# Kernel tuning notes

Measured on AMD Instinct MI355X. Metric: run time of the kernel, lower is better.

## Reference

```python
import jax, jax.numpy as jnp
import numpy as np

N = 50000
HID = 128
NH = 4
E_RES, E_SEQ, E_KNN = 100000, 100000, 200000
BN_EPS = 1e-5
NEG_SLOPE = 0.2


def _gat(h, src, dst, W, al, ar, resW, b):
    """DGL-style GATConv (eval mode: feat_drop off, residual=True, bias).
    h: (N, in), W/resW: (in, H*out), al/ar: (H, out), b: (H*out,)"""
    Hh, out = al.shape
    feat = (h @ W).reshape(N, Hh, out)                 # (N, H, out)
    el = jnp.sum(feat * al, axis=-1)                   # (N, H)
    er = jnp.sum(feat * ar, axis=-1)                   # (N, H)
    e = jax.nn.leaky_relu(el[src] + er[dst], NEG_SLOPE)  # (E, H)
    # edge softmax over incoming edges of each dst node (numerically stable)
    m = jax.ops.segment_max(e, dst, num_segments=N)    # (N, H)
    ex = jnp.exp(e - m[dst])
    s = jax.ops.segment_sum(ex, dst, num_segments=N)
    a = ex / s[dst]                                    # (E, H)
    msg = a[:, :, None] * feat[src]                    # (E, H, out)
    rst = jax.ops.segment_sum(msg, dst, num_segments=N)  # (N, H, out)
    return rst + (h @ resW).reshape(N, Hh, out) + b.reshape(1, Hh, out)


def _hetero(h, src_res, dst_res, src_seq, dst_seq, src_knn, dst_knn, W, al, ar, resW, b):
    # HeteroGraphConv with aggregate='sum' over relations, then mean over heads
    r = _gat(h, src_res, dst_res, W[0], al[0], ar[0], resW[0], b[0])
    r = r + _gat(h, src_seq, dst_seq, W[1], al[1], ar[1], resW[1], b[1])
    r = r + _gat(h, src_knn, dst_knn, W[2], al[2], ar[2], resW[2], b[2])
    return jnp.mean(r, axis=1)                         # (N, out)


def setup_inputs() -> dict:
    key = jax.random.key(0)
    ks = iter(jax.random.split(key, 32))
    inp = {}
    inp["x"] = jax.random.normal(next(ks), (N, HID), jnp.float32)
    inp["src_res"] = jax.random.randint(next(ks), (E_RES,), 0, N, jnp.int32)
    inp["dst_res"] = jax.random.randint(next(ks), (E_RES,), 0, N, jnp.int32)
    inp["src_seq"] = jax.random.randint(next(ks), (E_SEQ,), 0, N, jnp.int32)
    inp["dst_seq"] = jax.random.randint(next(ks), (E_SEQ,), 0, N, jnp.int32)
    inp["src_knn"] = jax.random.randint(next(ks), (E_KNN,), 0, N, jnp.int32)
    inp["dst_knn"] = jax.random.randint(next(ks), (E_KNN,), 0, N, jnp.int32)
    sc = 0.05
    for l in (0, 1):
        inp[f"W{l}"] = jax.random.normal(next(ks), (3, HID, NH * HID), jnp.float32) * sc
        inp[f"al{l}"] = jax.random.normal(next(ks), (3, NH, HID), jnp.float32) * sc
        inp[f"ar{l}"] = jax.random.normal(next(ks), (3, NH, HID), jnp.float32) * sc
        inp[f"resW{l}"] = jax.random.normal(next(ks), (3, HID, NH * HID), jnp.float32) * sc
        inp[f"b{l}"] = jax.random.normal(next(ks), (3, NH * HID), jnp.float32) * sc
    inp["fc_W"] = jax.random.normal(next(ks), (HID, HID), jnp.float32) * sc
    inp["fc_b"] = jax.random.normal(next(ks), (HID,), jnp.float32) * sc
    inp["bn_gamma"] = jnp.ones((HID,), jnp.float32)
    inp["bn_beta"] = jnp.zeros((HID,), jnp.float32)
    inp["bn_mean"] = jax.random.normal(next(ks), (HID,), jnp.float32) * sc
    inp["bn_var"] = jax.random.uniform(next(ks), (HID,), jnp.float32)
    return inp


def reference(x, src_res, dst_res, src_seq, dst_seq, src_knn, dst_knn,
              W0, al0, ar0, resW0, b0, W1, al1, ar1, resW1, b1,
              fc_W, fc_b, bn_gamma, bn_beta, bn_mean, bn_var):
    # layer 0: hetero GAT, head-mean, fc + ReLU + BatchNorm (eval), dropout=identity
    h = _hetero(x, src_res, dst_res, src_seq, dst_seq, src_knn, dst_knn,
                W0, al0, ar0, resW0, b0)
    h = jax.nn.relu(h @ fc_W + fc_b)
    h = (h - bn_mean) / jnp.sqrt(bn_var + BN_EPS) * bn_gamma + bn_beta
    # layer 1 (final): hetero GAT, head-mean
    out = _hetero(h, src_res, dst_res, src_seq, dst_seq, src_knn, dst_knn,
                  W1, al1, ar1, resW1, b1)
    return out
```

## Files before the change

kernel.cpp:

```cpp
#include <hip/hip_runtime.h>
#include <hip/hip_bf16.h>
#include <math.h>
#include <stdint.h>

#define NNODES 50000
#define SCHUNK 4096
#define AW 1664
#define XOFF 1536

typedef __bf16 bf16x8 __attribute__((ext_vector_type(8)));
typedef float f32x4 __attribute__((ext_vector_type(4)));
typedef unsigned short u16;
typedef unsigned int u32;

__device__ __forceinline__ float lrelu(float x){ return x >= 0.f ? x : 0.2f*x; }
__device__ __forceinline__ float lo2f(u32 v){ union{ u32 i; float f; } c; c.i = v<<16; return c.f; }
__device__ __forceinline__ float hi2f(u32 v){ union{ u32 i; float f; } c; c.i = v & 0xffff0000u; return c.f; }
__device__ __forceinline__ u16 f2b(float f){ __hip_bfloat16 h = __float2bfloat16(f); return *(u16*)&h; }
__device__ __forceinline__ u32 packbf(float a, float b){ return (u32)f2b(a) | ((u32)f2b(b) << 16); }

#define GLDS16(g, l) __builtin_amdgcn_global_load_lds( \
    (const __attribute__((address_space(1))) void*)(g), \
    (__attribute__((address_space(3))) void*)(l), 16, 0, 0)

__global__ void prep_all(const float* __restrict__ W0, const float* __restrict__ W1,
                         const float* __restrict__ resW0, const float* __restrict__ resW1,
                         const float* __restrict__ b0, const float* __restrict__ b1,
                         const float* __restrict__ al0, const float* __restrict__ ar0,
                         const float* __restrict__ al1, const float* __restrict__ ar1,
                         const float* __restrict__ fcW,
                         u16* __restrict__ Btb, float* __restrict__ biasf,
                         u16* __restrict__ wlb, u16* __restrict__ fcWtb)
{
    int gid = blockIdx.x*blockDim.x + threadIdx.x;
    if (gid < 2*128*AW){
        int l = gid / (128*AW);
        int rem = gid - l*(128*AW);
        int c = rem / AW;
        int j = rem - c*AW;
        const float* W  = l ? W1 : W0;
        const float* rw = l ? resW1 : resW0;
        float v;
        if (j < XOFF){
            int r = j >> 9, h = (j >> 7) & 3, k = j & 127;
            v = 0.25f * W[(size_t)r*65536 + (size_t)k*512 + h*128 + c];
        } else {
            int k = j - XOFF;
            float s = 0.f;
            for (int r = 0; r < 3; ++r)
                for (int h = 0; h < 4; ++h)
                    s += rw[(size_t)r*65536 + (size_t)k*512 + h*128 + c];
            v = 0.25f * s;
        }
        Btb[gid] = f2b(v);
    }
    if (gid < 256){
        int l = gid >> 7, c = gid & 127;
        const float* bb = l ? b1 : b0;
        float s = 0.f;
        for (int r = 0; r < 3; ++r)
            for (int h = 0; h < 4; ++h)
                s += bb[r*512 + h*128 + c];
        biasf[gid] = 0.25f*s;
    }
    if (gid < 2*128*128){
        int l = gid >> 14;
        int col = (gid >> 7) & 127;
        int k = gid & 127;
        float v = 0.f;
        if (col < 24){
            int r = col >> 3, lr = (col >> 2) & 1, h = col & 3;
            const float* W = l ? W1 : W0;
            const float* av = l ? (lr ? ar1 : al1) : (lr ? ar0 : al0);
            const float* wrow = W + (size_t)r*65536 + (size_t)k*512 + h*128;
            const float* arow = av + r*512 + h*128;
            for (int cc = 0; cc < 128; ++cc) v += wrow[cc]*arow[cc];
        }
        wlb[gid] = f2b(v);
    }
    if (gid < 128*128){
        int k = gid & 127, n = gid >> 7;
        fcWtb[gid] = f2b(fcW[k*128 + n]);
    }
}

__global__ __launch_bounds__(256) void xprep_kernel(const float* __restrict__ x,
    u16* __restrict__ Ax, const u16* __restrict__ wl, float* __restrict__ el, int M)
{
    __shared__ u16 Xs[64*136];
    __shared__ u16 Ws[32*136];
    const int tid = threadIdx.x;
    const int row0 = blockIdx.x*64;
    #pragma unroll
    for (int p = 0; p < 2; ++p){
        int idx = tid + p*256;
        int c = idx >> 4, kc = (idx & 15)*8;
        float4 v = make_float4(0.f,0.f,0.f,0.f);
        if (c < 24) v = *(const float4*)(wl + c*128 + kc);
        *(float4*)&Ws[c*136 + kc] = v;
    }
    int r = tid >> 2, cq = (tid & 3)*32;
    int grow = row0 + r;
    if (grow < M){
        #pragma unroll
        for (int i = 0; i < 8; ++i){
            float4 v = *(const float4*)(x + (size_t)grow*128 + cq + i*4);
            ushort4 o;
            o.x = f2b(v.x); o.y = f2b(v.y); o.z = f2b(v.z); o.w = f2b(v.w);
            *(ushort4*)(Ax + (size_t)grow*AW + cq + i*4) = o;
            *(ushort4*)&Xs[r*136 + cq + i*4] = o;
        }
    } else {
        ushort4 z; z.x=0; z.y=0; z.z=0; z.w=0;
        #pragma unroll
        for (int i = 0; i < 8; ++i) *(ushort4*)&Xs[r*136 + cq + i*4] = z;
    }
    __syncthreads();
    const int lane = tid & 63, wave = tid >> 6;
    const int r16 = lane & 15, quad = lane >> 4;
    f32x4 acc0 = {}, acc1 = {};
    #pragma unroll
    for (int ks = 0; ks < 4; ++ks){
        int ko = ks*32 + quad*8;
        bf16x8 a  = *(const bf16x8*)&Xs[(wave*16 + r16)*136 + ko];
        bf16x8 b0 = *(const bf16x8*)&Ws[r16*136 + ko];
        bf16x8 b1 = *(const bf16x8*)&Ws[(16 + r16)*136 + ko];
        acc0 = __builtin_amdgcn_mfma_f32_16x16x32_bf16(a, b0, acc0, 0,0,0);
        acc1 = __builtin_amdgcn_mfma_f32_16x16x32_bf16(a, b1, acc1, 0,0,0);
    }
    #pragma unroll
    for (int p = 0; p < 4; ++p){
        int row = row0 + wave*16 + quad*4 + p;
        if (row < M){
            el[(size_t)row*32 + r16] = acc0[p];
            if (r16 < 8) el[(size_t)row*32 + 16 + r16] = acc1[p];
        }
    }
}

__global__ void hist_all(const int* __restrict__ d0, const int* __restrict__ d1,
                         const int* __restrict__ d2, int e0, int e1, int e2,
                         int* __restrict__ cnt)
{
    int g = blockIdx.x*blockDim.x + threadIdx.x;
    if (g >= e0 + e1 + e2) return;
    int rel, idx;
    if (g < e0){ rel = 0; idx = g; }
    else if (g < e0 + e1){ rel = 1; idx = g - e0; }
    else { rel = 2; idx = g - e0 - e1; }
    const int* d = rel == 0 ? d0 : (rel == 1 ? d1 : d2);
    atomicAdd(cnt + (size_t)rel*NNODES + d[idx], 1);
}

__global__ __launch_bounds__(256) void scan_part(const int* __restrict__ cnt_all,
                                                 int* __restrict__ partials, int Nn, int nblk)
{
    int rel = blockIdx.y, blk = blockIdx.x;
    const int* cnt = cnt_all + (size_t)rel*Nn;
    int tid = threadIdx.x;
    int i0 = blk*SCHUNK + tid*16;
    int s = 0;
    #pragma unroll
    for (int k = 0; k < 4; ++k){
        int idx = i0 + k*4;
        if (idx + 3 < Nn){ int4 v = *(const int4*)(cnt + idx); s += v.x+v.y+v.z+v.w; }
        else { for (int j = 0; j < 4; ++j) if (idx+j < Nn) s += cnt[idx+j]; }
    }
    #pragma unroll
    for (int off = 1; off < 64; off <<= 1) s += __shfl_xor(s, off);
    __shared__ int ws[4];
    if ((tid & 63) == 0) ws[tid>>6] = s;
    __syncthreads();
    if (tid == 0) partials[rel*nblk + blk] = ws[0]+ws[1]+ws[2]+ws[3];
}

__global__ __launch_bounds__(256) void scan_write(const int* __restrict__ cnt_all,
                                                  const int* __restrict__ partials,
                                                  int* __restrict__ rp_all, int* __restrict__ cur_all,
                                                  int Nn, int nblk)
{
    int rel = blockIdx.y, blk = blockIdx.x;
    const int* cnt = cnt_all + (size_t)rel*Nn;
    int* rp  = rp_all  + (size_t)rel*(Nn+1);
    int* cur = cur_all + (size_t)rel*Nn;
    int tid = threadIdx.x;
    __shared__ int sOff;
    __shared__ int wsum[4];
    if (tid == 0){
        int o = 0;
        for (int b = 0; b < blk; ++b) o += partials[rel*nblk + b];
        sOff = o;
        if (blk == 0){
            int t = 0;
            for (int b = 0; b < nblk; ++b) t += partials[rel*nblk + b];
            rp[Nn] = t;
        }
    }
    int i0 = blk*SCHUNK + tid*16;
    int v[16];
    int s = 0;
    #pragma unroll
    for (int k = 0; k < 16; ++k){
        int idx = i0 + k;
        v[k] = (idx < Nn) ? cnt[idx] : 0;
        s += v[k];
    }
    int lane = tid & 63;
    int incl = s;
    #pragma unroll
    for (int off = 1; off < 64; off <<= 1){
        int t = __shfl_up(incl, off);
        if (lane >= off) incl += t;
    }
    if (lane == 63) wsum[tid>>6] = incl;
    __syncthreads();
    int woff = 0;
    for (int w = 0; w < (tid>>6); ++w) woff += wsum[w];
    int ex = sOff + woff + incl - s;
    #pragma unroll
    for (int k = 0; k < 16; ++k){
        int idx = i0 + k;
        if (idx < Nn){ rp[idx] = ex; cur[idx] = ex; }
        ex += v[k];
    }
}

__global__ void scatter_all(const int* __restrict__ s0, const int* __restrict__ s1,
                            const int* __restrict__ s2,
                            const int* __restrict__ d0, const int* __restrict__ d1,
                            const int* __restrict__ d2, int e0, int e1, int e2,
                            int* __restrict__ cur, int* __restrict__ colb,
                            int* __restrict__ dste)
{
    int g = blockIdx.x*blockDim.x + threadIdx.x;
    if (g >= e0 + e1 + e2) return;
    int rel, idx, coff;
    if (g < e0){ rel = 0; idx = g; coff = 0; }
    else if (g < e0 + e1){ rel = 1; idx = g - e0; coff = e0; }
    else { rel = 2; idx = g - e0 - e1; coff = e0 + e1; }
    const int* sp = rel == 0 ? s0 : (rel == 1 ? s1 : s2);
    const int* dp = rel == 0 ? d0 : (rel == 1 ? d1 : d2);
    int d = dp[idx];
    int pos = atomicAdd(cur + (size_t)rel*NNODES + d, 1);
    colb[coff + pos] = sp[idx];
    dste[coff + pos] = d;
}

__global__ void wprep(const int* __restrict__ colb, const int* __restrict__ dste,
                      int e0, int e01, int etot,
                      const float* __restrict__ el_all, uint4* __restrict__ rec)
{
    int j = blockIdx.x*blockDim.x + threadIdx.x;
    if (j >= etot) return;
    int rel = (j < e0) ? 0 : ((j < e01) ? 1 : 2);
    int src = colb[j], dst = dste[j];
    float4 es = *(const float4*)(el_all + (size_t)src*32 + rel*8);
    float4 ed = *(const float4*)(el_all + (size_t)dst*32 + rel*8 + 4);
    uint4 o;
    o.x = (u32)src;
    o.y = packbf(__expf(lrelu(es.x + ed.x)), __expf(lrelu(es.y + ed.y)));
    o.z = packbf(__expf(lrelu(es.z + ed.z)), __expf(lrelu(es.w + ed.w)));
    o.w = 0;
    rec[j] = o;
}

__global__ __launch_bounds__(256) void agg3(const int* __restrict__ rowp_all,
    const uint4* __restrict__ rec_all, int e0, int e01,
    const u16* __restrict__ Ax, u16* __restrict__ Abuf, int Nn)
{
    const int rel = blockIdx.y;
    const int tid = threadIdx.x;
    const int o = tid & 15;
    const int n = (blockIdx.x*256 + tid) >> 4;
    if (n >= Nn) return;
    const int* rowp = rowp_all + (size_t)rel*(Nn+1);
    const int coff = (rel == 0) ? 0 : ((rel == 1) ? e0 : e01);
    const uint4* rec = rec_all + coff;
    u16* op = Abuf + (size_t)n*AW + rel*512 + o*8;

    int beg = rowp[n], end = rowp[n+1];
    if (beg >= end){
        uint4 z; z.x = 0; z.y = 0; z.z = 0; z.w = 0;
        #pragma unroll
        for (int h = 0; h < 4; ++h) *(uint4*)(op + h*128) = z;
        return;
    }
    float acc[4][8] = {};
    float us0 = 0.f, us1 = 0.f, us2 = 0.f, us3 = 0.f;

    uint4 ra = rec[beg];
    uint4 xa = *(const uint4*)(Ax + (size_t)ra.x*AW + o*8);
    uint4 rb = ra, xb = xa;
    if (beg + 1 < end){
        rb = rec[beg+1];
        xb = *(const uint4*)(Ax + (size_t)rb.x*AW + o*8);
    }
    for (int j = beg; j < end; ++j){
        uint4 rc = rb, xc = xb;
        if (j + 2 < end){
            rc = rec[j+2];
            xc = *(const uint4*)(Ax + (size_t)rc.x*AW + o*8);
        }
        float w0 = lo2f(ra.y), w1 = hi2f(ra.y), w2 = lo2f(ra.z), w3 = hi2f(ra.z);
        us0 += w0; us1 += w1; us2 += w2; us3 += w3;
        float xv[8];
        xv[0] = lo2f(xa.x); xv[1] = hi2f(xa.x);
        xv[2] = lo2f(xa.y); xv[3] = hi2f(xa.y);
        xv[4] = lo2f(xa.z); xv[5] = hi2f(xa.z);
        xv[6] = lo2f(xa.w); xv[7] = hi2f(xa.w);
        #pragma unroll
        for (int c = 0; c < 8; ++c){
            acc[0][c] = fmaf(w0, xv[c], acc[0][c]);
            acc[1][c] = fmaf(w1, xv[c], acc[1][c]);
            acc[2][c] = fmaf(w2, xv[c], acc[2][c]);
            acc[3][c] = fmaf(w3, xv[c], acc[3][c]);
        }
        ra = rb; xa = xb; rb = rc; xb = xc;
    }
    float inv[4] = {1.f/us0, 1.f/us1, 1.f/us2, 1.f/us3};
    #pragma unroll
    for (int h = 0; h < 4; ++h){
        uint4 ov;
        ov.x = packbf(acc[h][0]*inv[h], acc[h][1]*inv[h]);
        ov.y = packbf(acc[h][2]*inv[h], acc[h][3]*inv[h]);
        ov.z = packbf(acc[h][4]*inv[h], acc[h][5]*inv[h]);
        ov.w = packbf(acc[h][6]*inv[h], acc[h][7]*inv[h]);
        *(uint4*)(op + h*128) = ov;
    }
}

template<int EPI, int FCF>
__global__ __launch_bounds__(256) void gemm_f(
    const u16* __restrict__ A, int Astride, int K,
    const u16* __restrict__ Bt,
    float* __restrict__ Cf, u16* __restrict__ Cb, int Cstride, int M,
    const float* __restrict__ bias, const float* __restrict__ gamma,
    const float* __restrict__ beta, const float* __restrict__ mean,
    const float* __restrict__ var,
    const u16* __restrict__ wl, float* __restrict__ el,
    const u16* __restrict__ fcw, const float* __restrict__ fcb2)
{
    __shared__ u16 smem[26112];
    const int tid = threadIdx.x;
    const int row0 = blockIdx.x*64;
    const int lane = tid & 63, wave = tid >> 6;
    const int wm = (wave >> 1)*32, wn = (wave & 1)*64;
    const int r16 = lane & 15, quad = lane >> 4;
    f32x4 acc[2][4] = {};

    const int r8 = lane >> 3, jc = lane & 7;
    const int soff = ((jc ^ r8) << 3);
    int gA0 = row0 + wave*16 + r8;      if (gA0 >= M) gA0 = M - 1;
    int gA1 = row0 + wave*16 + 8 + r8;  if (gA1 >= M) gA1 = M - 1;
    const u16* srcA0 = A + (size_t)gA0*Astride + soff;
    const u16* srcA1 = A + (size_t)gA1*Astride + soff;
    const u16* srcB0 = Bt + (size_t)(wave*32      + r8)*K + soff;
    const u16* srcB1 = Bt + (size_t)(wave*32 + 8  + r8)*K + soff;
    const u16* srcB2 = Bt + (size_t)(wave*32 + 16 + r8)*K + soff;
    const u16* srcB3 = Bt + (size_t)(wave*32 + 24 + r8)*K + soff;
    const int nk = K >> 6;
    const int swzbase = r16 & 7;

    #define STAGE(buf, k0) do { \
        u16* As_ = smem + (buf)*12288; \
        u16* Bs_ = As_ + 4096; \
        GLDS16(srcA0 + (k0), As_ + wave*1024); \
        GLDS16(srcA1 + (k0), As_ + wave*1024 + 512); \
        GLDS16(srcB0 + (k0), Bs_ + wave*2048); \
        GLDS16(srcB1 + (k0), Bs_ + wave*2048 + 512); \
        GLDS16(srcB2 + (k0), Bs_ + wave*2048 + 1024); \
        GLDS16(srcB3 + (k0), Bs_ + wave*2048 + 1536); \
    } while (0)

    STAGE(0, 0);
    __syncthreads();
    for (int t = 0; t < nk; ++t){
        int cur = t & 1;
        if (t + 1 < nk) STAGE(cur ^ 1, (t + 1) << 6);
        const u16* As = smem + cur*12288;
        const u16* Bs = As + 4096;
        #pragma unroll
        for (int ks = 0; ks < 2; ++ks){
            int swz = ((ks*4 + quad) ^ swzbase) << 3;
            bf16x8 a0 = *(const bf16x8*)&As[(wm + r16)*64 + swz];
            bf16x8 a1 = *(const bf16x8*)&As[(wm + 16 + r16)*64 + swz];
            #pragma unroll
            for (int j = 0; j < 4; ++j){
                bf16x8 b = *(const bf16x8*)&Bs[(wn + j*16 + r16)*64 + swz];
                acc[0][j] = __builtin_amdgcn_mfma_f32_16x16x32_bf16(a0, b, acc[0][j], 0,0,0);
                acc[1][j] = __builtin_amdgcn_mfma_f32_16x16x32_bf16(a1, b, acc[1][j], 0,0,0);
            }
        }
        __syncthreads();
    }
    #undef STAGE

    u16* Cs = smem;
    u16* Ws = smem + 64*136;

    if (!FCF){
        #pragma unroll
        for (int i = 0; i < 2; ++i){
            #pragma unroll
            for (int p = 0; p < 4; ++p){
                int row = row0 + wm + i*16 + quad*4 + p;
                #pragma unroll
                for (int j = 0; j < 4; ++j){
                    int col = wn + j*16 + r16;
                    float v = acc[i][j][p] + bias[col];
                    if (row < M){
                        if (EPI == 1) Cf[(size_t)row*Cstride + col] = v;
                        else          Cb[(size_t)row*Cstride + col] = f2b(v);
                    }
                }
            }
        }
    } else {
        #pragma unroll
        for (int i = 0; i < 2; ++i){
            #pragma unroll
            for (int p = 0; p < 4; ++p){
                int rl = wm + i*16 + quad*4 + p;
                #pragma unroll
                for (int j = 0; j < 4; ++j){
                    int col = wn + j*16 + r16;
                    Cs[rl*136 + col] = f2b(acc[i][j][p] + bias[col]);
                }
            }
        }
        #pragma unroll
        for (int p = 0; p < 8; ++p){
            int idx = tid + p*256;
            int n = idx >> 4, kc = (idx & 15)*8;
            *(float4*)&Ws[n*136 + kc] = *(const float4*)(fcw + n*128 + kc);
        }
        __syncthreads();
        f32x4 fa[8] = {};
        #pragma unroll
        for (int ks = 0; ks < 4; ++ks){
            int ko = ks*32 + quad*8;
            bf16x8 a = *(const bf16x8*)&Cs[(wave*16 + r16)*136 + ko];
            #pragma unroll
            for (int j = 0; j < 8; ++j){
                bf16x8 b = *(const bf16x8*)&Ws[(j*16 + r16)*136 + ko];
                fa[j] = __builtin_amdgcn_mfma_f32_16x16x32_bf16(a, b, fa[j], 0,0,0);
            }
        }
        __syncthreads();
        #pragma unroll
        for (int j = 0; j < 8; ++j){
            int col = j*16 + r16;
            float fb = fcb2[col];
            float mn = mean[col];
            float sc = gamma[col]*rsqrtf(var[col] + 1e-5f);
            float bt = beta[col];
            #pragma unroll
            for (int p = 0; p < 4; ++p){
                int rl = wave*16 + quad*4 + p;
                int row = row0 + rl;
                float v = fa[j][p] + fb;
                v = fmaxf(v, 0.f);
                v = (v - mn)*sc + bt;
                u16 vb = f2b(v);
                if (row < M) Cb[(size_t)row*Cstride + col] = vb;
                Cs[rl*136 + col] = vb;
            }
        }
        #pragma unroll
        for (int p = 0; p < 2; ++p){
            int idx = tid + p*256;
            int c = idx >> 4, kc = (idx & 15)*8;
            float4 v = make_float4(0.f,0.f,0.f,0.f);
            if (c < 24) v = *(const float4*)(wl + c*128 + kc);
            *(float4*)&Ws[c*136 + kc] = v;
        }
        __syncthreads();
        f32x4 e0 = {}, e1 = {};
        #pragma unroll
        for (int ks = 0; ks < 4; ++ks){
            int ko = ks*32 + quad*8;
            bf16x8 a  = *(const bf16x8*)&Cs[(wave*16 + r16)*136 + ko];
            bf16x8 b0 = *(const bf16x8*)&Ws[r16*136 + ko];
            bf16x8 b1 = *(const bf16x8*)&Ws[(16 + r16)*136 + ko];
            e0 = __builtin_amdgcn_mfma_f32_16x16x32_bf16(a, b0, e0, 0,0,0);
            e1 = __builtin_amdgcn_mfma_f32_16x16x32_bf16(a, b1, e1, 0,0,0);
        }
        #pragma unroll
        for (int p = 0; p < 4; ++p){
            int row = row0 + wave*16 + quad*4 + p;
            if (row < M){
                el[(size_t)row*32 + r16] = e0[p];
                if (r16 < 8) el[(size_t)row*32 + 16 + r16] = e1[p];
            }
        }
    }
}

static inline char* align256(char* p){ return (char*)(((uintptr_t)p + 255) & ~(uintptr_t)255); }

extern "C" void kernel_launch(void* const* d_in, const int* in_sizes, int n_in,
                              void* d_out, int out_size, void* d_ws, size_t ws_size,
                              hipStream_t stream)
{
    const float* x      = (const float*)d_in[0];
    const int* srcs[3]  = {(const int*)d_in[1], (const int*)d_in[3], (const int*)d_in[5]};
    const int* dsts[3]  = {(const int*)d_in[2], (const int*)d_in[4], (const int*)d_in[6]};
    const int  E[3]     = {in_sizes[1], in_sizes[3], in_sizes[5]};
    const float* W0     = (const float*)d_in[7];
    const float* al0    = (const float*)d_in[8];
    const float* ar0    = (const float*)d_in[9];
    const float* resW0  = (const float*)d_in[10];
    const float* b0     = (const float*)d_in[11];
    const float* W1     = (const float*)d_in[12];
    const float* al1    = (const float*)d_in[13];
    const float* ar1    = (const float*)d_in[14];
    const float* resW1  = (const float*)d_in[15];
    const float* b1     = (const float*)d_in[16];
    const float* fcW    = (const float*)d_in[17];
    const float* fcb    = (const float*)d_in[18];
    const float* gamma  = (const float*)d_in[19];
    const float* beta   = (const float*)d_in[20];
    const float* bmean  = (const float*)d_in[21];
    const float* bvar   = (const float*)d_in[22];
    float* out = (float*)d_out;

    char* p = (char*)d_ws;
    u16*   Abuf  = (u16*)p;   p += (size_t)NNODES*AW*2;    p = align256(p);
    float* el    = (float*)p; p += (size_t)NNODES*32*4;    p = align256(p);
    int*   cnt   = (int*)p;   p += (size_t)3*NNODES*4;     p = align256(p);
    int*   rowp  = (int*)p;   p += (size_t)3*(NNODES+1)*4; p = align256(p);
    int*   cur   = (int*)p;   p += (size_t)3*NNODES*4;     p = align256(p);
    int*   colb  = (int*)p;   p += (size_t)(E[0]+E[1]+E[2])*4; p = align256(p);
    int*   dste  = (int*)p;   p += (size_t)(E[0]+E[1]+E[2])*4; p = align256(p);
    uint4* rec   = (uint4*)p; p += (size_t)(E[0]+E[1]+E[2])*16; p = align256(p);
    u16*   Btb   = (u16*)p;   p += (size_t)2*128*AW*2;     p = align256(p);
    u16*   wlb   = (u16*)p;   p += (size_t)2*128*128*2;    p = align256(p);
    u16*   fcWtb = (u16*)p;   p += (size_t)128*128*2;      p = align256(p);
    float* biasf = (float*)p; p += (size_t)2*128*4;        p = align256(p);
    int*   parts = (int*)p;   p += (size_t)3*64*4;

    const int NBLK = (NNODES + SCHUNK - 1)/SCHUNK;
    const int MB = (NNODES + 63)/64;
    const int AGGBLKS = (NNODES*16 + 255)/256;
    const int ETOT = E[0] + E[1] + E[2];
    dim3 blk(256);
    u16* Ax = Abuf + XOFF;

    hipMemsetAsync(cnt, 0, (size_t)3*NNODES*sizeof(int), stream);
    prep_all<<<(2*128*AW + 255)/256, blk, 0, stream>>>(W0, W1, resW0, resW1, b0, b1,
                                                       al0, ar0, al1, ar1, fcW,
                                                       Btb, biasf, wlb, fcWtb);
    xprep_kernel<<<MB, blk, 0, stream>>>(x, Ax, wlb, el, NNODES);
    hist_all<<<(ETOT + 255)/256, blk, 0, stream>>>(dsts[0], dsts[1], dsts[2], E[0], E[1], E[2], cnt);
    scan_part <<<dim3(NBLK,3), blk, 0, stream>>>(cnt, parts, NNODES, NBLK);
    scan_write<<<dim3(NBLK,3), blk, 0, stream>>>(cnt, parts, rowp, cur, NNODES, NBLK);
    scatter_all<<<(ETOT + 255)/256, blk, 0, stream>>>(srcs[0], srcs[1], srcs[2],
                                                      dsts[0], dsts[1], dsts[2],
                                                      E[0], E[1], E[2], cur, colb, dste);

    wprep<<<(ETOT + 255)/256, blk, 0, stream>>>(colb, dste, E[0], E[0]+E[1], ETOT, el, rec);
    agg3<<<dim3(AGGBLKS,3), blk, 0, stream>>>(rowp, rec, E[0], E[0]+E[1], Ax, Abuf, NNODES);
    gemm_f<0,1><<<MB, blk, 0, stream>>>(Abuf, AW, AW, Btb, nullptr, Ax, AW, NNODES,
                                        biasf, gamma, beta, bmean, bvar,
                                        wlb + 16384, el, fcWtb, fcb);

    wprep<<<(ETOT + 255)/256, blk, 0, stream>>>(colb, dste, E[0], E[0]+E[1], ETOT, el, rec);
    agg3<<<dim3(AGGBLKS,3), blk, 0, stream>>>(rowp, rec, E[0], E[0]+E[1], Ax, Abuf, NNODES);
    gemm_f<1,0><<<MB, blk, 0, stream>>>(Abuf, AW, AW, Btb + (size_t)128*AW, out, nullptr, 128, NNODES,
                                        biasf + 128, nullptr, nullptr, nullptr, nullptr,
                                        nullptr, nullptr, nullptr, nullptr);
}
```

Before: 380.0 us.

## Enlarge GEMM row tile to 128 with single-buffered LDS and fold memset into prep

The fused GEMM now computes a 128-row tile per block with a 4x4 MFMA accumulator per wave, which doubles A/B reuse from LDS and halves the number of blocks. The double-buffered prefetch is replaced by a single buffer with a load-then-sync pattern, and the launch bounds ask for 3 blocks per SM. The FC epilogue now processes the weights in two halves to fit LDS. The separate memset of the histogram counters is folded into the prep kernel to drop one launch. The trade-off is that global-to-LDS loads no longer overlap with MFMA work, and larger per-wave register use may limit occupancy.

```diff
diff --git a/kernel.cpp b/kernel.cpp
--- a/kernel.cpp
+++ b/kernel.cpp
@@ -30,9 +30,11 @@
                          const float* __restrict__ al1, const float* __restrict__ ar1,
                          const float* __restrict__ fcW,
                          u16* __restrict__ Btb, float* __restrict__ biasf,
-                         u16* __restrict__ wlb, u16* __restrict__ fcWtb)
+                         u16* __restrict__ wlb, u16* __restrict__ fcWtb,
+                         int* __restrict__ cnt)
 {
     int gid = blockIdx.x*blockDim.x + threadIdx.x;
+    if (gid < 3*NNODES) cnt[gid] = 0;
     if (gid < 2*128*AW){
         int l = gid / (128*AW);
         int rem = gid - l*(128*AW);
@@ -330,7 +332,7 @@
 }
 
 template<int EPI, int FCF>
-__global__ __launch_bounds__(256) void gemm_f(
+__global__ __launch_bounds__(256, 3) void gemm_f(
     const u16* __restrict__ A, int Astride, int K,
     const u16* __restrict__ Bt,
     float* __restrict__ Cf, u16* __restrict__ Cb, int Cstride, int M,
@@ -340,67 +342,58 @@
     const u16* __restrict__ wl, float* __restrict__ el,
     const u16* __restrict__ fcw, const float* __restrict__ fcb2)
 {
-    __shared__ u16 smem[26112];
+    __shared__ u16 smem[FCF ? 26112 : 16384];
     const int tid = threadIdx.x;
-    const int row0 = blockIdx.x*64;
+    const int row0 = blockIdx.x*128;
     const int lane = tid & 63, wave = tid >> 6;
-    const int wm = (wave >> 1)*32, wn = (wave & 1)*64;
+    const int wm = (wave >> 1)*64, wn = (wave & 1)*64;
     const int r16 = lane & 15, quad = lane >> 4;
-    f32x4 acc[2][4] = {};
+    const int swzbase = r16 & 7;
+    f32x4 acc[4][4] = {};
 
     const int r8 = lane >> 3, jc = lane & 7;
     const int soff = ((jc ^ r8) << 3);
-    int gA0 = row0 + wave*16 + r8;      if (gA0 >= M) gA0 = M - 1;
-    int gA1 = row0 + wave*16 + 8 + r8;  if (gA1 >= M) gA1 = M - 1;
-    const u16* srcA0 = A + (size_t)gA0*Astride + soff;
-    const u16* srcA1 = A + (size_t)gA1*Astride + soff;
-    const u16* srcB0 = Bt + (size_t)(wave*32      + r8)*K + soff;
-    const u16* srcB1 = Bt + (size_t)(wave*32 + 8  + r8)*K + soff;
-    const u16* srcB2 = Bt + (size_t)(wave*32 + 16 + r8)*K + soff;
-    const u16* srcB3 = Bt + (size_t)(wave*32 + 24 + r8)*K + soff;
+    const u16* srcA[4];
+    const u16* srcB[4];
+    #pragma unroll
+    for (int g = 0; g < 4; ++g){
+        int gr = row0 + wave*32 + g*8 + r8;
+        if (gr >= M) gr = M - 1;
+        srcA[g] = A + (size_t)gr*Astride + soff;
+        srcB[g] = Bt + (size_t)(wave*32 + g*8 + r8)*K + soff;
+    }
+    u16* As = smem;
+    u16* Bs = smem + 8192;
     const int nk = K >> 6;
-    const int swzbase = r16 & 7;
-
-    #define STAGE(buf, k0) do { \
-        u16* As_ = smem + (buf)*12288; \
-        u16* Bs_ = As_ + 4096; \
-        GLDS16(srcA0 + (k0), As_ + wave*1024); \
-        GLDS16(srcA1 + (k0), As_ + wave*1024 + 512); \
-        GLDS16(srcB0 + (k0), Bs_ + wave*2048); \
-        GLDS16(srcB1 + (k0), Bs_ + wave*2048 + 512); \
-        GLDS16(srcB2 + (k0), Bs_ + wave*2048 + 1024); \
-        GLDS16(srcB3 + (k0), Bs_ + wave*2048 + 1536); \
-    } while (0)
-
-    STAGE(0, 0);
-    __syncthreads();
+
     for (int t = 0; t < nk; ++t){
-        int cur = t & 1;
-        if (t + 1 < nk) STAGE(cur ^ 1, (t + 1) << 6);
-        const u16* As = smem + cur*12288;
-        const u16* Bs = As + 4096;
+        const int k0 = t << 6;
+        #pragma unroll
+        for (int g = 0; g < 4; ++g){
+            GLDS16(srcA[g] + k0, As + wave*2048 + g*512);
+            GLDS16(srcB[g] + k0, Bs + wave*2048 + g*512);
+        }
+        __syncthreads();
         #pragma unroll
         for (int ks = 0; ks < 2; ++ks){
             int swz = ((ks*4 + quad) ^ swzbase) << 3;
-            bf16x8 a0 = *(const bf16x8*)&As[(wm + r16)*64 + swz];
-            bf16x8 a1 = *(const bf16x8*)&As[(wm + 16 + r16)*64 + swz];
-            #pragma unroll
-            for (int j = 0; j < 4; ++j){
-                bf16x8 b = *(const bf16x8*)&Bs[(wn + j*16 + r16)*64 + swz];
-                acc[0][j] = __builtin_amdgcn_mfma_f32_16x16x32_bf16(a0, b, acc[0][j], 0,0,0);
-                acc[1][j] = __builtin_amdgcn_mfma_f32_16x16x32_bf16(a1, b, acc[1][j], 0,0,0);
-            }
+            bf16x8 a[4], b[4];
+            #pragma unroll
+            for (int i = 0; i < 4; ++i) a[i] = *(const bf16x8*)&As[(wm + i*16 + r16)*64 + swz];
+            #pragma unroll
+            for (int j = 0; j < 4; ++j) b[j] = *(const bf16x8*)&Bs[(wn + j*16 + r16)*64 + swz];
+            #pragma unroll
+            for (int i = 0; i < 4; ++i)
+                #pragma unroll
+                for (int j = 0; j < 4; ++j)
+                    acc[i][j] = __builtin_amdgcn_mfma_f32_16x16x32_bf16(a[i], b[j], acc[i][j], 0,0,0);
         }
         __syncthreads();
     }
-    #undef STAGE
-
-    u16* Cs = smem;
-    u16* Ws = smem + 64*136;
 
     if (!FCF){
         #pragma unroll
-        for (int i = 0; i < 2; ++i){
+        for (int i = 0; i < 4; ++i){
             #pragma unroll
             for (int p = 0; p < 4; ++p){
                 int row = row0 + wm + i*16 + quad*4 + p;
@@ -416,8 +409,10 @@
             }
         }
     } else {
-        #pragma unroll
-        for (int i = 0; i < 2; ++i){
+        u16* Cs = smem;
+        u16* Ws = smem + 17408;
+        #pragma unroll
+        for (int i = 0; i < 4; ++i){
             #pragma unroll
             for (int p = 0; p < 4; ++p){
                 int rl = wm + i*16 + quad*4 + p;
@@ -428,42 +423,53 @@
                 }
             }
         }
-        #pragma unroll
-        for (int p = 0; p < 8; ++p){
-            int idx = tid + p*256;
-            int n = idx >> 4, kc = (idx & 15)*8;
-            *(float4*)&Ws[n*136 + kc] = *(const float4*)(fcw + n*128 + kc);
-        }
         __syncthreads();
-        f32x4 fa[8] = {};
-        #pragma unroll
-        for (int ks = 0; ks < 4; ++ks){
-            int ko = ks*32 + quad*8;
-            bf16x8 a = *(const bf16x8*)&Cs[(wave*16 + r16)*136 + ko];
-            #pragma unroll
-            for (int j = 0; j < 8; ++j){
-                bf16x8 b = *(const bf16x8*)&Ws[(j*16 + r16)*136 + ko];
-                fa[j] = __builtin_amdgcn_mfma_f32_16x16x32_bf16(a, b, fa[j], 0,0,0);
-            }
-        }
-        __syncthreads();
-        #pragma unroll
-        for (int j = 0; j < 8; ++j){
-            int col = j*16 + r16;
+        f32x4 fa[2][8] = {};
+        #pragma unroll
+        for (int hh = 0; hh < 2; ++hh){
+            {
+                int rr = tid >> 2, sg = (tid & 3)*32;
+                const u16* src = fcw + (size_t)(hh*64 + rr)*128 + sg;
+                #pragma unroll
+                for (int q = 0; q < 4; ++q)
+                    *(float4*)&Ws[rr*136 + sg + q*8] = *(const float4*)(src + q*8);
+            }
+            __syncthreads();
+            #pragma unroll
+            for (int ks = 0; ks < 4; ++ks){
+                int ko = ks*32 + quad*8;
+                #pragma unroll
+                for (int i = 0; i < 2; ++i){
+                    bf16x8 a = *(const bf16x8*)&Cs[(wave*32 + i*16 + r16)*136 + ko];
+                    #pragma unroll
+                    for (int jj = 0; jj < 4; ++jj){
+                        bf16x8 b = *(const bf16x8*)&Ws[(jj*16 + r16)*136 + ko];
+                        fa[i][hh*4+jj] = __builtin_amdgcn_mfma_f32_16x16x32_bf16(a, b, fa[i][hh*4+jj], 0,0,0);
+                    }
+                }
+            }
+            __syncthreads();
+        }
+        #pragma unroll
+        for (int f = 0; f < 8; ++f){
+            int col = f*16 + r16;
             float fb = fcb2[col];
             float mn = mean[col];
             float sc = gamma[col]*rsqrtf(var[col] + 1e-5f);
             float bt = beta[col];
             #pragma unroll
-            for (int p = 0; p < 4; ++p){
-                int rl = wave*16 + quad*4 + p;
-                int row = row0 + rl;
-                float v = fa[j][p] + fb;
-                v = fmaxf(v, 0.f);
-                v = (v - mn)*sc + bt;
-                u16 vb = f2b(v);
-                if (row < M) Cb[(size_t)row*Cstride + col] = vb;
-                Cs[rl*136 + col] = vb;
+            for (int i = 0; i < 2; ++i){
+                #pragma unroll
+                for (int p = 0; p < 4; ++p){
+                    int rl = wave*32 + i*16 + quad*4 + p;
+                    int row = row0 + rl;
+                    float v = fa[i][f][p] + fb;
+                    v = fmaxf(v, 0.f);
+                    v = (v - mn)*sc + bt;
+                    u16 vb = f2b(v);
+                    if (row < M) Cb[(size_t)row*Cstride + col] = vb;
+                    Cs[rl*136 + col] = vb;
+                }
             }
         }
         #pragma unroll
@@ -475,22 +481,28 @@
             *(float4*)&Ws[c*136 + kc] = v;
         }
         __syncthreads();
-        f32x4 e0 = {}, e1 = {};
+        f32x4 e0[2] = {}, e1[2] = {};
         #pragma unroll
         for (int ks = 0; ks < 4; ++ks){
             int ko = ks*32 + quad*8;
-            bf16x8 a  = *(const bf16x8*)&Cs[(wave*16 + r16)*136 + ko];
-            bf16x8 b0 = *(const bf16x8*)&Ws[r16*136 + ko];
-            bf16x8 b1 = *(const bf16x8*)&Ws[(16 + r16)*136 + ko];
-            e0 = __builtin_amdgcn_mfma_f32_16x16x32_bf16(a, b0, e0, 0,0,0);
-            e1 = __builtin_amdgcn_mfma_f32_16x16x32_bf16(a, b1, e1, 0,0,0);
-        }
-        #pragma unroll
-        for (int p = 0; p < 4; ++p){
-            int row = row0 + wave*16 + quad*4 + p;
-            if (row < M){
-                el[(size_t)row*32 + r16] = e0[p];
-                if (r16 < 8) el[(size_t)row*32 + 16 + r16] = e1[p];
+            #pragma unroll
+            for (int i = 0; i < 2; ++i){
+                bf16x8 a  = *(const bf16x8*)&Cs[(wave*32 + i*16 + r16)*136 + ko];
+                bf16x8 b0 = *(const bf16x8*)&Ws[r16*136 + ko];
+                bf16x8 b1 = *(const bf16x8*)&Ws[(16 + r16)*136 + ko];
+                e0[i] = __builtin_amdgcn_mfma_f32_16x16x32_bf16(a, b0, e0[i], 0,0,0);
+                e1[i] = __builtin_amdgcn_mfma_f32_16x16x32_bf16(a, b1, e1[i], 0,0,0);
+            }
+        }
+        #pragma unroll
+        for (int i = 0; i < 2; ++i){
+            #pragma unroll
+            for (int p = 0; p < 4; ++p){
+                int row = row0 + wave*32 + i*16 + quad*4 + p;
+                if (row < M){
+                    el[(size_t)row*32 + r16] = e0[i][p];
+                    if (r16 < 8) el[(size_t)row*32 + 16 + r16] = e1[i][p];
+                }
             }
         }
     }
@@ -540,17 +552,17 @@
     int*   parts = (int*)p;   p += (size_t)3*64*4;
 
     const int NBLK = (NNODES + SCHUNK - 1)/SCHUNK;
-    const int MB = (NNODES + 63)/64;
+    const int MB64 = (NNODES + 63)/64;
+    const int MBG  = (NNODES + 127)/128;
     const int AGGBLKS = (NNODES*16 + 255)/256;
     const int ETOT = E[0] + E[1] + E[2];
     dim3 blk(256);
     u16* Ax = Abuf + XOFF;
 
-    hipMemsetAsync(cnt, 0, (size_t)3*NNODES*sizeof(int), stream);
     prep_all<<<(2*128*AW + 255)/256, blk, 0, stream>>>(W0, W1, resW0, resW1, b0, b1,
                                                        al0, ar0, al1, ar1, fcW,
-                                                       Btb, biasf, wlb, fcWtb);
-    xprep_kernel<<<MB, blk, 0, stream>>>(x, Ax, wlb, el, NNODES);
+                                                       Btb, biasf, wlb, fcWtb, cnt);
+    xprep_kernel<<<MB64, blk, 0, stream>>>(x, Ax, wlb, el, NNODES);
     hist_all<<<(ETOT + 255)/256, blk, 0, stream>>>(dsts[0], dsts[1], dsts[2], E[0], E[1], E[2], cnt);
     scan_part <<<dim3(NBLK,3), blk, 0, stream>>>(cnt, parts, NNODES, NBLK);
     scan_write<<<dim3(NBLK,3), blk, 0, stream>>>(cnt, parts, rowp, cur, NNODES, NBLK);
@@ -560,13 +572,13 @@
 
     wprep<<<(ETOT + 255)/256, blk, 0, stream>>>(colb, dste, E[0], E[0]+E[1], ETOT, el, rec);
     agg3<<<dim3(AGGBLKS,3), blk, 0, stream>>>(rowp, rec, E[0], E[0]+E[1], Ax, Abuf, NNODES);
-    gemm_f<0,1><<<MB, blk, 0, stream>>>(Abuf, AW, AW, Btb, nullptr, Ax, AW, NNODES,
-                                        biasf, gamma, beta, bmean, bvar,
-                                        wlb + 16384, el, fcWtb, fcb);
+    gemm_f<0,1><<<MBG, blk, 0, stream>>>(Abuf, AW, AW, Btb, nullptr, Ax, AW, NNODES,
+                                         biasf, gamma, beta, bmean, bvar,
+                                         wlb + 16384, el, fcWtb, fcb);
 
     wprep<<<(ETOT + 255)/256, blk, 0, stream>>>(colb, dste, E[0], E[0]+E[1], ETOT, el, rec);
     agg3<<<dim3(AGGBLKS,3), blk, 0, stream>>>(rowp, rec, E[0], E[0]+E[1], Ax, Abuf, NNODES);
-    gemm_f<1,0><<<MB, blk, 0, stream>>>(Abuf, AW, AW, Btb + (size_t)128*AW, out, nullptr, 128, NNODES,
-                                        biasf + 128, nullptr, nullptr, nullptr, nullptr,
-                                        nullptr, nullptr, nullptr, nullptr);
-}
+    gemm_f<1,0><<<MBG, blk, 0, stream>>>(Abuf, AW, AW, Btb + (size_t)128*AW, out, nullptr, 128, NNODES,
+                                         biasf + 128, nullptr, nullptr, nullptr, nullptr,
+                                         nullptr, nullptr, nullptr, nullptr);
+}
```

Result: faster. 361.3 us (-4.9%).
